# Kernel optimization log

Measured on AMD Instinct MI355X. Metric: run time of the kernel, lower is better.

The kernel has to match this reference:

```python
import jax, jax.numpy as jnp
import numpy as np
import math

B, S, D = 4, 2048, 2048
NH, NKV, HD = 16, 4, 128

def setup_inputs() -> dict:
    key = jax.random.key(0)
    ks = jax.random.split(key, 9)
    s = 1.0 / math.sqrt(D)
    return {
        "x": jax.random.normal(ks[0], (B, S, D), dtype=jnp.float32),
        "Wq": jax.random.normal(ks[1], (D, NH * HD), dtype=jnp.float32) * s,
        "bq": jnp.zeros((NH * HD,), dtype=jnp.float32),
        "Wk": jax.random.normal(ks[2], (D, NKV * HD), dtype=jnp.float32) * s,
        "bk": jnp.zeros((NKV * HD,), dtype=jnp.float32),
        "Wv": jax.random.normal(ks[3], (D, NKV * HD), dtype=jnp.float32) * s,
        "bv": jnp.zeros((NKV * HD,), dtype=jnp.float32),
        "Wo": jax.random.normal(ks[4], (D, D), dtype=jnp.float32) * s,
        "bo": jnp.zeros((D,), dtype=jnp.float32),
    }

def reference(x, Wq, bq, Wk, bk, Wv, bv, Wo, bo):
    b, s, _ = x.shape
    group = NH // NKV
    q = (x @ Wq + bq).reshape(b, s, NH, HD).transpose(0, 2, 1, 3)   # [B,NH,S,HD]
    k = (x @ Wk + bk).reshape(b, s, NKV, HD).transpose(0, 2, 1, 3)  # [B,NKV,S,HD]
    v = (x @ Wv + bv).reshape(b, s, NKV, HD).transpose(0, 2, 1, 3)
    # repeat_interleave KV heads to match query heads
    k = jnp.repeat(k, group, axis=1)  # [B,NH,S,HD]
    v = jnp.repeat(v, group, axis=1)
    scores = jnp.einsum("bhqd,bhkd->bhqk", q, k) / math.sqrt(HD)
    causal = jnp.tril(jnp.ones((s, s), dtype=bool))
    scores = jnp.where(causal, scores, -jnp.inf)
    probs = jax.nn.softmax(scores, axis=-1)  # dropout p=0.0 -> identity
    out = jnp.einsum("bhqk,bhkd->bhqd", probs, v)
    out = out.transpose(0, 2, 1, 3).reshape(b, s, NH * HD)
    return out @ Wo + bo
```

## Files before the change

### kernel.cpp

```cpp
#include <hip/hip_runtime.h>
#include <hip/hip_bf16.h>

typedef __attribute__((ext_vector_type(4)))  float f32x4;
typedef __attribute__((ext_vector_type(16))) float f32x16;
typedef __attribute__((ext_vector_type(8)))  short s16x8;
typedef __attribute__((ext_vector_type(4)))  short s16x4;
typedef __attribute__((ext_vector_type(4)))  float fvec4;

__device__ __forceinline__ short f2bf(float f) {
    union { float f; unsigned u; } x; x.f = f;
    unsigned r = x.u + 0x7fffu + ((x.u >> 16) & 1u);
    return (short)(r >> 16);
}

__device__ __forceinline__ void gload_lds16(const short* g, short* lds) {
    __builtin_amdgcn_global_load_lds(
        (const __attribute__((address_space(1))) void*)g,
        (__attribute__((address_space(3))) void*)lds, 16, 0, 0);
}

__global__ __launch_bounds__(256) void convert_bf16(const float* __restrict__ X,
                                                    short* __restrict__ Y) {
    size_t i = ((size_t)blockIdx.x * 256 + threadIdx.x) * 8;
    fvec4 a = *(const fvec4*)&X[i];
    fvec4 b = *(const fvec4*)&X[i + 4];
    s16x8 o;
    o[0] = f2bf(a[0]); o[1] = f2bf(a[1]); o[2] = f2bf(a[2]); o[3] = f2bf(a[3]);
    o[4] = f2bf(b[0]); o[5] = f2bf(b[1]); o[6] = f2bf(b[2]); o[7] = f2bf(b[3]);
    *(s16x8*)&Y[i] = o;
}

__global__ __launch_bounds__(256) void tconv(const float* __restrict__ W,
                                             short* __restrict__ Wt,
                                             int K, int N) {
    __shared__ float tile[32][33];
    const int k0 = blockIdx.x * 32, n0 = blockIdx.y * 32;
    const int tx = threadIdx.x & 31, ty = threadIdx.x >> 5;
    #pragma unroll
    for (int i = 0; i < 4; ++i) {
        int k = ty + i * 8;
        tile[k][tx] = W[(size_t)(k0 + k) * N + n0 + tx];
    }
    __syncthreads();
    #pragma unroll
    for (int i = 0; i < 4; ++i) {
        int n = ty + i * 8;
        Wt[(size_t)(n0 + n) * K + k0 + tx] = f2bf(tile[tx][n]);
    }
}

template<int MODE>
__global__ __launch_bounds__(256) void gemm_bt(const short* __restrict__ A,
                                               const short* __restrict__ Bt,
                                               const float* __restrict__ bias,
                                               void* __restrict__ Cv,
                                               int M, int N, int K) {
    __shared__ __align__(16) short As[128 * 64];
    __shared__ __align__(16) short Bs[128 * 64];
    const int tid = threadIdx.x, lane = tid & 63, wid = tid >> 6;
    const int wr = wid >> 1, wc = wid & 1;
    const int lr = lane & 15, g = lane >> 4;
    const int m0 = blockIdx.y * 128, n0 = blockIdx.x * 128;
    const int r8 = lane >> 3, c8 = lane & 7;

    f32x4 acc[4][4] = {};

    const short* ga = A  + (size_t)(m0 + wid * 8 + r8) * K + c8 * 8;
    const short* gb = Bt + (size_t)(n0 + wid * 8 + r8) * K + c8 * 8;

    for (int k0 = 0; k0 < K; k0 += 64) {
        #pragma unroll
        for (int it = 0; it < 4; ++it) {
            gload_lds16(ga + (size_t)(it * 32) * K + k0, &As[(wid * 8 + it * 32) * 64]);
            gload_lds16(gb + (size_t)(it * 32) * K + k0, &Bs[(wid * 8 + it * 32) * 64]);
        }
        __syncthreads();
        #pragma unroll
        for (int kk = 0; kk < 2; ++kk) {
            s16x8 af[4], bfv[4];
            #pragma unroll
            for (int m = 0; m < 4; ++m)
                af[m] = *(const s16x8*)&As[(wr * 64 + m * 16 + lr) * 64 + kk * 32 + g * 8];
            #pragma unroll
            for (int n = 0; n < 4; ++n)
                bfv[n] = *(const s16x8*)&Bs[(wc * 64 + n * 16 + lr) * 64 + kk * 32 + g * 8];
            #pragma unroll
            for (int m = 0; m < 4; ++m)
                #pragma unroll
                for (int n = 0; n < 4; ++n)
                    acc[m][n] = __builtin_amdgcn_mfma_f32_16x16x32_bf16(af[m], bfv[n], acc[m][n], 0, 0, 0);
        }
        __syncthreads();
    }
    #pragma unroll
    for (int m = 0; m < 4; ++m) {
        if constexpr (MODE == 2) {
            #pragma unroll
            for (int n = 0; n < 4; ++n) {
                int col = n0 + wc * 64 + n * 16 + lr;
                int kvh = col >> 7, d = col & 127;
                int row0 = m0 + wr * 64 + m * 16 + g * 4;
                int b = row0 >> 11, s0 = row0 & 2047;
                int s0p = (s0 & ~15) | (((s0 >> 2) & 1) << 3) | (((s0 >> 3) & 1) << 2);
                s16x4 o;
                #pragma unroll
                for (int j = 0; j < 4; ++j) o[j] = f2bf(acc[m][n][j] + bias[col]);
                *(s16x4*)&((short*)Cv)[(((size_t)b * 4 + kvh) * 128 + d) * 2048 + s0p] = o;
            }
        } else {
            #pragma unroll
            for (int j = 0; j < 4; ++j) {
                int row = m0 + wr * 64 + m * 16 + g * 4 + j;
                #pragma unroll
                for (int n = 0; n < 4; ++n) {
                    int col = n0 + wc * 64 + n * 16 + lr;
                    float v = acc[m][n][j] + bias[col];
                    ((short*)Cv)[(size_t)row * N + col] = f2bf(v);
                }
            }
        }
    }
}

template<int MODE>
__global__ __launch_bounds__(512, 1) void gemm256(const short* __restrict__ A,
                                                  const short* __restrict__ Bt,
                                                  const float* __restrict__ bias,
                                                  void* __restrict__ Cv,
                                                  int M, int N, int K) {
    __shared__ __align__(16) short As[2][16384];
    __shared__ __align__(16) short Bs[2][16384];
    const int tid = threadIdx.x, lane = tid & 63, w = tid >> 6;
    const int wr = w >> 2, wc = w & 3;
    const int lr = lane & 15, g = lane >> 4;
    const int m0 = blockIdx.y * 256, n0 = blockIdx.x * 256;
    const int r0 = w * 8 + (lane >> 3);
    const int sw = ((lane & 7) ^ ((lane >> 3) & 7)) * 8;
    const int swr = lr & 7;

    const short* ga = A  + (size_t)(m0 + r0) * K + sw;
    const short* gb = Bt + (size_t)(n0 + r0) * K + sw;

    f32x4 acc[8][4] = {};
    const int NT = K >> 6;

#define STAGE256(d, t) do {                                                     \
    const int kk0_ = (t) << 6;                                                  \
    _Pragma("unroll")                                                           \
    for (int it_ = 0; it_ < 4; ++it_) {                                         \
        gload_lds16(ga + (size_t)(it_ * 64) * K + kk0_, &As[d][it_ * 4096 + w * 512]); \
        gload_lds16(gb + (size_t)(it_ * 64) * K + kk0_, &Bs[d][it_ * 4096 + w * 512]); \
    }                                                                           \
} while (0)

    STAGE256(0, 0);

    for (int T = 0; T < NT; ++T) {
        const int d = T & 1;
        if (T + 1 < NT) {
            STAGE256((T + 1) & 1, T + 1);
            asm volatile("s_waitcnt vmcnt(8)" ::: "memory");
        } else {
            asm volatile("s_waitcnt vmcnt(0)" ::: "memory");
        }
        __builtin_amdgcn_s_barrier();
        __builtin_amdgcn_sched_barrier(0);
        s16x8 bf[4][2];
        #pragma unroll
        for (int n = 0; n < 4; ++n)
            #pragma unroll
            for (int kk = 0; kk < 2; ++kk)
                bf[n][kk] = *(const s16x8*)&Bs[d][(wc * 64 + n * 16 + lr) * 64 +
                                                 (((kk << 2) | g) ^ swr) * 8];
        #pragma unroll
        for (int p = 0; p < 4; ++p) {
            s16x8 af[2][2];
            #pragma unroll
            for (int mm = 0; mm < 2; ++mm)
                #pragma unroll
                for (int kk = 0; kk < 2; ++kk)
                    af[mm][kk] = *(const s16x8*)&As[d][(wr * 128 + (p * 2 + mm) * 16 + lr) * 64 +
                                                      (((kk << 2) | g) ^ swr) * 8];
            __builtin_amdgcn_s_setprio(1);
            #pragma unroll
            for (int kk = 0; kk < 2; ++kk)
                #pragma unroll
                for (int mm = 0; mm < 2; ++mm)
                    #pragma unroll
                    for (int n = 0; n < 4; ++n)
                        acc[p * 2 + mm][n] = __builtin_amdgcn_mfma_f32_16x16x32_bf16(
                            af[mm][kk], bf[n][kk], acc[p * 2 + mm][n], 0, 0, 0);
            __builtin_amdgcn_s_setprio(0);
            __builtin_amdgcn_s_barrier();
        }
        __builtin_amdgcn_sched_barrier(0);
    }
    #pragma unroll
    for (int m = 0; m < 8; ++m)
        #pragma unroll
        for (int j = 0; j < 4; ++j) {
            int row = m0 + wr * 128 + m * 16 + g * 4 + j;
            #pragma unroll
            for (int n = 0; n < 4; ++n) {
                int col = n0 + wc * 64 + n * 16 + lr;
                float v = acc[m][n][j] + bias[col];
                if constexpr (MODE == 1) ((short*)Cv)[(size_t)row * N + col] = f2bf(v);
                else                     ((float*)Cv)[(size_t)row * N + col] = v;
            }
        }
#undef STAGE256
}

#define SC2 0.12751743f

__global__ __launch_bounds__(512, 1) void attn_kernel(const short* __restrict__ Q,
                                                      const short* __restrict__ Kg,
                                                      const short* __restrict__ Vtg,
                                                      short* __restrict__ Oa) {
    __shared__ __align__(16) short Klds[2][8192];
    __shared__ __align__(16) short Vlds[2][8192];
    const int tid = threadIdx.x;
    const int lane = tid & 63, w = tid >> 6;
    const int l31 = lane & 31, hi = lane >> 5, e7 = lane & 7;
    const int ve = hi ^ e7;

    const int bid = blockIdx.x;
    const int phase = bid >> 8, idx = bid & 255;
    const int bh = idx >> 2;
    const int b = bh >> 4, h = bh & 15;
    const int qt = phase ? (3 - (idx & 3)) : (4 + (idx & 3));
    const int qb = qt << 8;
    const int kvh = h >> 2;

    const int q_min = qb + w * 32;
    const int qg = q_min + l31;
    const size_t qrow = (size_t)b * 2048 + qg;

    s16x8 qf[8];
    #pragma unroll
    for (int c = 0; c < 8; ++c)
        qf[c] = *(const s16x8*)&Q[qrow * 2048 + h * 128 + c * 16 + hi * 8];

    f32x16 oacc[4] = {};
    float m_run = -1e28f, l_run = 0.f;

    const int nt = (qb >> 6) + 4;

    const short* Kbase = Kg + ((size_t)b * 2048) * 512 + kvh * 128;
    const short* Vbase = Vtg + ((size_t)(b * 4 + kvh)) * 128 * 2048;

    const int krow0 = w * 4 + (lane >> 4), kslot = lane & 15;
    const int vrow0 = w * 8 + (lane >> 3), vslot = lane & 7;

#define STAGE(buf, t) do {                                                        \
    const int kv0_ = (t) << 6;                                                    \
    _Pragma("unroll")                                                             \
    for (int s_ = 0; s_ < 2; ++s_) {                                              \
        int kr = s_ * 32 + krow0;                                                 \
        gload_lds16(Kbase + (size_t)(kv0_ + kr) * 512 + (kslot ^ (kr & 7)) * 8,   \
                    &Klds[buf][s_ * 4096 + w * 512]);                             \
        int vr = s_ * 64 + vrow0;                                                 \
        gload_lds16(Vbase + (size_t)vr * 2048 + kv0_ + (vslot ^ (vr & 7)) * 8,    \
                    &Vlds[buf][s_ * 4096 + w * 512]);                             \
    }                                                                             \
} while (0)

    STAGE(0, 0);
    __syncthreads();

    int cur = 0;
    for (int t = 0; t < nt; ++t) {
        if (t + 1 < nt) STAGE(cur ^ 1, t + 1);
        #pragma unroll
        for (int st = 0; st < 2; ++st) {
            const int kvoff = (t << 6) + (st << 5);
            if (kvoff > q_min) break;
            f32x16 s = {};
            const short* kb = &Klds[cur][((st << 5) + l31) * 128];
            #pragma unroll
            for (int c = 0; c < 8; ++c) {
                s16x8 kf = *(const s16x8*)&kb[(((c << 1) ^ ve)) * 8];
                s = __builtin_amdgcn_mfma_f32_32x32x16_bf16(kf, qf[c], s, 0, 0, 0);
            }
            if (kvoff == q_min) {
                #pragma unroll
                for (int r = 0; r < 16; ++r) {
                    const int rw = (r & 3) + 8 * (r >> 2) + 4 * hi;
                    if (rw > l31) s[r] = -1e30f;
                }
            }
            float m01 = fmaxf(s[0], s[1]),   m23 = fmaxf(s[2], s[3]);
            float m45 = fmaxf(s[4], s[5]),   m67 = fmaxf(s[6], s[7]);
            float m89 = fmaxf(s[8], s[9]),   mab = fmaxf(s[10], s[11]);
            float mcd = fmaxf(s[12], s[13]), mef = fmaxf(s[14], s[15]);
            float mA = fmaxf(fmaxf(m01, m23), fmaxf(m45, m67));
            float mB = fmaxf(fmaxf(m89, mab), fmaxf(mcd, mef));
            float pm = fmaxf(mA, mB);
            pm = fmaxf(pm, __shfl_xor(pm, 32));
            if (!__all(pm <= m_run + 90.5f)) {
                float mn = fmaxf(m_run, pm);
                float fs = __builtin_amdgcn_exp2f((m_run - mn) * SC2);
                l_run *= fs;
                #pragma unroll
                for (int dn = 0; dn < 4; ++dn)
                    #pragma unroll
                    for (int r = 0; r < 16; ++r) oacc[dn][r] *= fs;
                m_run = mn;
            }
            const float mb2 = m_run * SC2;
            #pragma unroll
            for (int r = 0; r < 16; ++r)
                s[r] = __builtin_amdgcn_exp2f(fmaf(s[r], SC2, -mb2));
            float s01 = s[0] + s[1],   s23 = s[2] + s[3];
            float s45 = s[4] + s[5],   s67 = s[6] + s[7];
            float s89 = s[8] + s[9],   sab = s[10] + s[11];
            float scd = s[12] + s[13], sef = s[14] + s[15];
            float sAB = ((s01 + s23) + (s45 + s67)) + ((s89 + sab) + (scd + sef));
            l_run += sAB + __shfl_xor(sAB, 32);
            s16x8 pa0, pa1;
            #pragma unroll
            for (int j = 0; j < 8; ++j) { pa0[j] = f2bf(s[j]); pa1[j] = f2bf(s[8 + j]); }
            const short* vb = &Vlds[cur][l31 * 64];
            #pragma unroll
            for (int dn = 0; dn < 4; ++dn) {
                s16x8 vf = *(const s16x8*)&vb[dn * 2048 + (((st << 2) ^ ve)) * 8];
                oacc[dn] = __builtin_amdgcn_mfma_f32_32x32x16_bf16(vf, pa0, oacc[dn], 0, 0, 0);
            }
            #pragma unroll
            for (int dn = 0; dn < 4; ++dn) {
                s16x8 vf = *(const s16x8*)&vb[dn * 2048 + ((((st << 2) | 2) ^ ve)) * 8];
                oacc[dn] = __builtin_amdgcn_mfma_f32_32x32x16_bf16(vf, pa1, oacc[dn], 0, 0, 0);
            }
        }
        __syncthreads();
        cur ^= 1;
    }
    const float inv = 1.0f / l_run;
    const size_t obase = qrow * 2048 + h * 128;
    #pragma unroll
    for (int dn = 0; dn < 4; ++dn)
        #pragma unroll
        for (int u = 0; u < 4; ++u) {
            s16x4 o;
            #pragma unroll
            for (int j = 0; j < 4; ++j) o[j] = f2bf(oacc[dn][u * 4 + j] * inv);
            *(s16x4*)&Oa[obase + dn * 32 + u * 8 + hi * 4] = o;
        }
#undef STAGE
}

extern "C" void kernel_launch(void* const* d_in, const int* in_sizes, int n_in,
                              void* d_out, int out_size, void* d_ws, size_t ws_size,
                              hipStream_t stream) {
    const float* x  = (const float*)d_in[0];
    const float* Wq = (const float*)d_in[1];
    const float* bq = (const float*)d_in[2];
    const float* Wk = (const float*)d_in[3];
    const float* bk = (const float*)d_in[4];
    const float* Wv = (const float*)d_in[5];
    const float* bv = (const float*)d_in[6];
    const float* Wo = (const float*)d_in[7];
    const float* bo = (const float*)d_in[8];
    float* out = (float*)d_out;

    char* ws = (char*)d_ws;
    short* Xb  = (short*)(ws);
    short* Qb  = (short*)(ws + (size_t)33554432);
    short* Kb  = (short*)(ws + (size_t)67108864);
    short* Vt  = (short*)(ws + (size_t)75497472);
    short* WoT = (short*)(ws);
    char* dob = (char*)d_out;
    short* WqT = (short*)(dob);
    short* WkT = (short*)(dob + (size_t)8388608);
    short* WvT = (short*)(dob + (size_t)10485760);

    const int M = 8192, D = 2048;

    convert_bf16<<<dim3((M * D) / (256 * 8)), 256, 0, stream>>>(x, Xb);
    tconv<<<dim3(64, 64), 256, 0, stream>>>(Wq, WqT, D, D);
    tconv<<<dim3(64, 16), 256, 0, stream>>>(Wk, WkT, D, 512);
    tconv<<<dim3(64, 16), 256, 0, stream>>>(Wv, WvT, D, 512);

    gemm256<1><<<dim3(8, 32), 512, 0, stream>>>(Xb, WqT, bq, Qb, M, 2048, D);
    gemm_bt<1><<<dim3(4, 64), 256, 0, stream>>>(Xb, WkT, bk, Kb, M, 512, D);
    gemm_bt<2><<<dim3(4, 64), 256, 0, stream>>>(Xb, WvT, bv, Vt, M, 512, D);

    tconv<<<dim3(64, 64), 256, 0, stream>>>(Wo, WoT, D, D);

    attn_kernel<<<dim3(512), 512, 0, stream>>>(Qb, Kb, Vt, Qb);

    gemm256<0><<<dim3(8, 32), 512, 0, stream>>>(Qb, WoT, bo, out, M, 2048, D);
}
```

Measured before the change: 387.8 us.

## Fuse K/V projections, remap GEMM and attention blocks for XCD L2 locality

Merges the separate K and V projection GEMMs into one launch over a concatenated transposed weight, with the epilogue branching on column range. The 256-tile GEMMs and the attention kernel now map a 1D block index so that blocks sharing A rows or the same KV head land on the same XCD, aiming to improve L2 reuse across the chiplets. The attention kernel also switches the bf16 conversion to the HIP intrinsic. The block remapping assumes round-robin dispatch of blocks across 8 XCDs.

After: 327.8 us. 15.5% less time.

```diff
diff --git a/kernel.cpp b/kernel.cpp
--- a/kernel.cpp
+++ b/kernel.cpp
@@ -11,6 +11,11 @@
     union { float f; unsigned u; } x; x.f = f;
     unsigned r = x.u + 0x7fffu + ((x.u >> 16) & 1u);
     return (short)(r >> 16);
+}
+
+__device__ __forceinline__ short cvtbf(float f) {
+    __hip_bfloat16 t = __float2bfloat16(f);
+    return *reinterpret_cast<short*>(&t);
 }
 
 __device__ __forceinline__ void gload_lds16(const short* g, short* lds) {
@@ -49,11 +54,12 @@
     }
 }
 
-template<int MODE>
-__global__ __launch_bounds__(256) void gemm_bt(const short* __restrict__ A,
+__global__ __launch_bounds__(256) void gemm_kv(const short* __restrict__ A,
                                                const short* __restrict__ Bt,
-                                               const float* __restrict__ bias,
-                                               void* __restrict__ Cv,
+                                               const float* __restrict__ bias_k,
+                                               const float* __restrict__ bias_v,
+                                               short* __restrict__ Kout,
+                                               short* __restrict__ Vout,
                                                int M, int N, int K) {
     __shared__ __align__(16) short As[128 * 64];
     __shared__ __align__(16) short Bs[128 * 64];
@@ -92,33 +98,33 @@
         }
         __syncthreads();
     }
-    #pragma unroll
-    for (int m = 0; m < 4; ++m) {
-        if constexpr (MODE == 2) {
+    if (n0 < 512) {
+        #pragma unroll
+        for (int m = 0; m < 4; ++m)
+            #pragma unroll
+            for (int j = 0; j < 4; ++j) {
+                int row = m0 + wr * 64 + m * 16 + g * 4 + j;
+                #pragma unroll
+                for (int n = 0; n < 4; ++n) {
+                    int col = n0 + wc * 64 + n * 16 + lr;
+                    Kout[(size_t)row * 512 + col] = f2bf(acc[m][n][j] + bias_k[col]);
+                }
+            }
+    } else {
+        #pragma unroll
+        for (int m = 0; m < 4; ++m)
             #pragma unroll
             for (int n = 0; n < 4; ++n) {
-                int col = n0 + wc * 64 + n * 16 + lr;
-                int kvh = col >> 7, d = col & 127;
+                int vcol = n0 - 512 + wc * 64 + n * 16 + lr;
+                int kvh = vcol >> 7, d = vcol & 127;
                 int row0 = m0 + wr * 64 + m * 16 + g * 4;
                 int b = row0 >> 11, s0 = row0 & 2047;
                 int s0p = (s0 & ~15) | (((s0 >> 2) & 1) << 3) | (((s0 >> 3) & 1) << 2);
                 s16x4 o;
                 #pragma unroll
-                for (int j = 0; j < 4; ++j) o[j] = f2bf(acc[m][n][j] + bias[col]);
-                *(s16x4*)&((short*)Cv)[(((size_t)b * 4 + kvh) * 128 + d) * 2048 + s0p] = o;
-            }
-        } else {
-            #pragma unroll
-            for (int j = 0; j < 4; ++j) {
-                int row = m0 + wr * 64 + m * 16 + g * 4 + j;
-                #pragma unroll
-                for (int n = 0; n < 4; ++n) {
-                    int col = n0 + wc * 64 + n * 16 + lr;
-                    float v = acc[m][n][j] + bias[col];
-                    ((short*)Cv)[(size_t)row * N + col] = f2bf(v);
-                }
-            }
-        }
+                for (int j = 0; j < 4; ++j) o[j] = f2bf(acc[m][n][j] + bias_v[vcol]);
+                *(s16x4*)&Vout[(((size_t)b * 4 + kvh) * 128 + d) * 2048 + s0p] = o;
+            }
     }
 }
 
@@ -133,7 +139,10 @@
     const int tid = threadIdx.x, lane = tid & 63, w = tid >> 6;
     const int wr = w >> 2, wc = w & 3;
     const int lr = lane & 15, g = lane >> 4;
-    const int m0 = blockIdx.y * 256, n0 = blockIdx.x * 256;
+    const int bid = blockIdx.x;
+    const int xcd = bid & 7, ii = bid >> 3;
+    const int m0 = (xcd * 4 + (ii & 3)) * 256;
+    const int n0 = (ii >> 2) * 256;
     const int r0 = w * 8 + (lane >> 3);
     const int sw = ((lane & 7) ^ ((lane >> 3) & 7)) * 8;
     const int swr = lr & 7;
@@ -225,12 +234,12 @@
     const int ve = hi ^ e7;
 
     const int bid = blockIdx.x;
-    const int phase = bid >> 8, idx = bid & 255;
-    const int bh = idx >> 2;
-    const int b = bh >> 4, h = bh & 15;
-    const int qt = phase ? (3 - (idx & 3)) : (4 + (idx & 3));
+    const int grp = bid & 15, j = bid >> 4;
+    const int b = grp >> 2, kvh = grp & 3;
+    const int h = kvh * 4 + (j & 3);
+    const int qtp = (j >> 2) & 3, ph = j >> 4;
+    const int qt = ph ? (3 - qtp) : (4 + qtp);
     const int qb = qt << 8;
-    const int kvh = h >> 2;
 
     const int q_min = qb + w * 32;
     const int qg = q_min + l31;
@@ -319,7 +328,7 @@
             l_run += sAB + __shfl_xor(sAB, 32);
             s16x8 pa0, pa1;
             #pragma unroll
-            for (int j = 0; j < 8; ++j) { pa0[j] = f2bf(s[j]); pa1[j] = f2bf(s[8 + j]); }
+            for (int jj = 0; jj < 8; ++jj) { pa0[jj] = cvtbf(s[jj]); pa1[jj] = cvtbf(s[8 + jj]); }
             const short* vb = &Vlds[cur][l31 * 64];
             #pragma unroll
             for (int dn = 0; dn < 4; ++dn) {
@@ -343,7 +352,7 @@
         for (int u = 0; u < 4; ++u) {
             s16x4 o;
             #pragma unroll
-            for (int j = 0; j < 4; ++j) o[j] = f2bf(oacc[dn][u * 4 + j] * inv);
+            for (int jj = 0; jj < 4; ++jj) o[jj] = cvtbf(oacc[dn][u * 4 + jj] * inv);
             *(s16x4*)&Oa[obase + dn * 32 + u * 8 + hi * 4] = o;
         }
 #undef STAGE
@@ -370,24 +379,22 @@
     short* Vt  = (short*)(ws + (size_t)75497472);
     short* WoT = (short*)(ws);
     char* dob = (char*)d_out;
-    short* WqT = (short*)(dob);
-    short* WkT = (short*)(dob + (size_t)8388608);
-    short* WvT = (short*)(dob + (size_t)10485760);
+    short* WqT  = (short*)(dob);
+    short* WkvT = (short*)(dob + (size_t)8388608);
 
     const int M = 8192, D = 2048;
 
     convert_bf16<<<dim3((M * D) / (256 * 8)), 256, 0, stream>>>(x, Xb);
     tconv<<<dim3(64, 64), 256, 0, stream>>>(Wq, WqT, D, D);
-    tconv<<<dim3(64, 16), 256, 0, stream>>>(Wk, WkT, D, 512);
-    tconv<<<dim3(64, 16), 256, 0, stream>>>(Wv, WvT, D, 512);
-
-    gemm256<1><<<dim3(8, 32), 512, 0, stream>>>(Xb, WqT, bq, Qb, M, 2048, D);
-    gemm_bt<1><<<dim3(4, 64), 256, 0, stream>>>(Xb, WkT, bk, Kb, M, 512, D);
-    gemm_bt<2><<<dim3(4, 64), 256, 0, stream>>>(Xb, WvT, bv, Vt, M, 512, D);
+    tconv<<<dim3(64, 16), 256, 0, stream>>>(Wk, WkvT, D, 512);
+    tconv<<<dim3(64, 16), 256, 0, stream>>>(Wv, WkvT + (size_t)512 * D, D, 512);
+
+    gemm256<1><<<dim3(256), 512, 0, stream>>>(Xb, WqT, bq, Qb, M, 2048, D);
+    gemm_kv<<<dim3(8, 64), 256, 0, stream>>>(Xb, WkvT, bk, bv, Kb, Vt, M, 1024, D);
 
     tconv<<<dim3(64, 64), 256, 0, stream>>>(Wo, WoT, D, D);
 
     attn_kernel<<<dim3(512), 512, 0, stream>>>(Qb, Kb, Vt, Qb);
 
-    gemm256<0><<<dim3(8, 32), 512, 0, stream>>>(Qb, WoT, bo, out, M, 2048, D);
-}
+    gemm256<0><<<dim3(256), 512, 0, stream>>>(Qb, WoT, bo, out, M, 2048, D);
+}
```
